# Kernel tuning notes

Hardware: AMD Instinct MI355X
Metric: run time of the kernel (lower is better)

Reference implementation:

```python
import jax, jax.numpy as jnp
import numpy as np

N, D, K = 16384, 512, 8192  # tokens, embed_dim, n_embed


def setup_inputs() -> dict:
    key = jax.random.key(0)
    k1, k2 = jax.random.split(key)
    xs = jax.random.normal(k1, (N, D), dtype=jnp.float32)
    embed_weight = jax.random.normal(k2, (K, D), dtype=jnp.float32)
    return {"xs": xs, "embed_weight": embed_weight}


def reference(xs, embed_weight):
    distance = ((xs ** 2).sum(axis=1, keepdims=True)
                + (embed_weight ** 2).sum(axis=1)
                - 2.0 * jnp.matmul(xs, embed_weight.T))
    indices = jnp.argmin(distance, axis=1)           # [N]
    output = embed_weight[indices]                   # gather -> [N, D]
    # straight-through estimator
    output_x = xs + jax.lax.stop_gradient(output - xs)
    e_latent_loss = jnp.mean((jax.lax.stop_gradient(output) - xs) ** 2)
    q_latent_loss = jnp.mean((output - jax.lax.stop_gradient(xs)) ** 2)
    loss = q_latent_loss + 0.25 * e_latent_loss
    return output_x, loss
```

## Files before the change

### kernel.cpp

```cpp
#include <hip/hip_runtime.h>
#include <stdint.h>

#define N_TOK   16384
#define DIM     512
#define K_CODES 8192
#define BM      128
#define BN      256
#define BK      32
#define NCHUNK  32
#define MU      0.25f

typedef __attribute__((ext_vector_type(8))) _Float16 f16x8;
typedef __attribute__((ext_vector_type(4))) _Float16 f16x4;
typedef __attribute__((ext_vector_type(4))) float f32x4;
typedef __attribute__((ext_vector_type(2))) unsigned long long u64x2;

__device__ __forceinline__ unsigned int fmono(float f) {
  unsigned int b = __float_as_uint(f);
  unsigned int mask = ((int)b < 0) ? 0xFFFFFFFFu : 0x80000000u;
  return b ^ mask;
}
__device__ __forceinline__ float finv(unsigned int m) {
  return (m & 0x80000000u) ? __uint_as_float(m ^ 0x80000000u)
                           : __uint_as_float(~m);
}
__device__ __forceinline__ void async16(const void* gptr, void* lptr) {
  __builtin_amdgcn_global_load_lds(
      (const __attribute__((address_space(1))) unsigned int*)gptr,
      (__attribute__((address_space(3))) unsigned int*)lptr,
      16, 0, 0);
}
__device__ __forceinline__ unsigned long long shflx(unsigned long long v, int x) {
  const int lo = __shfl_xor((int)(unsigned int)v, x, 64);
  const int hi = __shfl_xor((int)(unsigned int)(v >> 32), x, 64);
  return ((unsigned long long)(unsigned int)hi << 32) | (unsigned int)lo;
}
__device__ __forceinline__ unsigned long long umin64(unsigned long long a,
                                                     unsigned long long b) {
  return a < b ? a : b;
}
__device__ __forceinline__ unsigned long long umax64(unsigned long long a,
                                                     unsigned long long b) {
  return a < b ? b : a;
}

__global__ __launch_bounds__(256) void castx_kernel(
    const float* __restrict__ in, _Float16* __restrict__ out) {
  const int gid = blockIdx.x * 256 + threadIdx.x;
  const float4 v = ((const float4*)in)[gid];
  f16x4 h;
  h.x = (_Float16)v.x; h.y = (_Float16)v.y;
  h.z = (_Float16)v.z; h.w = (_Float16)v.w;
  *(f16x4*)(out + (size_t)gid * 4) = h;
}

__global__ __launch_bounds__(256) void enorm_cast_kernel(
    const float* __restrict__ ew, float* __restrict__ enorm,
    _Float16* __restrict__ E16) {
  const int lane = threadIdx.x & 63;
  const int wid  = threadIdx.x >> 6;
  const int row  = blockIdx.x * 4 + wid;
  const float4 v0 = *(const float4*)(ew + (size_t)row * DIM + lane * 8);
  const float4 v1 = *(const float4*)(ew + (size_t)row * DIM + lane * 8 + 4);
  const float f[8] = {v0.x, v0.y, v0.z, v0.w, v1.x, v1.y, v1.z, v1.w};
  f16x8 h;
  double s = 0.0;
#pragma unroll
  for (int k = 0; k < 8; ++k) {
    s = fma((double)f[k], (double)f[k], s);
    h[k] = (_Float16)f[k];
  }
  *(f16x8*)(E16 + (size_t)row * DIM + lane * 8) = h;
#pragma unroll
  for (int off = 32; off > 0; off >>= 1) s += __shfl_down(s, off, 64);
  if (lane == 0) enorm[row] = (float)s;
}

__global__ __launch_bounds__(256) void gemm_top2_kernel(
    const _Float16* __restrict__ X16,
    const _Float16* __restrict__ E16,
    const float* __restrict__ enorm,
    unsigned long long* __restrict__ buf1,
    unsigned long long* __restrict__ buf2) {
  __shared__ __align__(16) union {
    _Float16 buf[2][12288];
    unsigned long long mg[BM][16][2];
  } sh;

  const int tid  = threadIdx.x;
  const int lane = tid & 63;
  const int wid  = tid >> 6;
  const int quad = lane >> 4;
  const int l15  = lane & 15;

  const int row0  = blockIdx.y * BM;
  const int nbase = blockIdx.x * BN;

  const int wm = (wid >> 1) * 64;
  const int wn = (wid & 1) * 128;

  const int issue0 = wid * 6;
  const int srow   = lane >> 2;
  const int schunk = (lane & 3) ^ ((lane >> 3) & 3);

  auto STAGE = [&](int p, int k0) {
    char* base = (char*)(&sh.buf[p][0]);
#pragma unroll
    for (int q = 0; q < 6; ++q) {
      const int issue = issue0 + q;
      if (issue < 8) {
        const int r = issue * 16 + srow;
        async16(X16 + (size_t)(row0 + r) * DIM + k0 + schunk * 8,
                base + issue * 1024);
      } else {
        const int bi = issue - 8;
        const int r = bi * 16 + srow;
        async16(E16 + (size_t)(nbase + r) * DIM + k0 + schunk * 8,
                base + 8192 + bi * 1024);
      }
    }
  };

  f32x4 acc[4][8];
#pragma unroll
  for (int i = 0; i < 4; ++i)
#pragma unroll
    for (int j = 0; j < 8; ++j) acc[i][j] = (f32x4){0.f, 0.f, 0.f, 0.f};

  STAGE(0, 0);
  __syncthreads();

  for (int ks = 0; ks < DIM / BK; ++ks) {
    const int p = ks & 1;
    if (ks < DIM / BK - 1) STAGE(p ^ 1, (ks + 1) * BK);

    const char* baseA = (const char*)(&sh.buf[p][0]);
    const char* baseB = baseA + 8192;
    f16x8 a[4];
#pragma unroll
    for (int i = 0; i < 4; ++i) {
      const int ra = wm + i * 16 + l15;
      a[i] = *(const f16x8*)(baseA + ra * 64 + ((quad ^ ((ra >> 1) & 3)) * 16));
    }
#pragma unroll
    for (int jh = 0; jh < 2; ++jh) {
      f16x8 b[4];
#pragma unroll
      for (int jj = 0; jj < 4; ++jj) {
        const int rb = wn + (jh * 4 + jj) * 16 + l15;
        b[jj] = *(const f16x8*)(baseB + rb * 64 + ((quad ^ ((rb >> 1) & 3)) * 16));
      }
#pragma unroll
      for (int i = 0; i < 4; ++i)
#pragma unroll
        for (int jj = 0; jj < 4; ++jj)
          acc[i][jh * 4 + jj] = __builtin_amdgcn_mfma_f32_16x16x32_f16(
              a[i], b[jj], acc[i][jh * 4 + jj], 0, 0, 0);
    }
    __syncthreads();
  }

  float en8[8];
#pragma unroll
  for (int j = 0; j < 8; ++j) en8[j] = enorm[nbase + wn + j * 16 + l15];
  const unsigned int ngb = (unsigned int)(nbase + wn + l15);

#pragma unroll
  for (int i = 0; i < 4; ++i) {
    const int mrow = wm + i * 16 + quad * 4;
#pragma unroll
    for (int r = 0; r < 4; ++r) {
      float b1 = __builtin_inff(), b2v = __builtin_inff();
      unsigned int b1i = 0u, b2i = 0u;
#pragma unroll
      for (int j = 0; j < 8; ++j) {
        const float v = fmaf(-2.f, acc[i][j][r], en8[j]);
        const unsigned int ng = ngb + j * 16;
        if (v < b1) { b2v = b1; b2i = b1i; b1 = v; b1i = ng; }
        else if (v < b2v) { b2v = v; b2i = ng; }
      }
      unsigned long long p1 =
          ((unsigned long long)fmono(b1) << 32) | (unsigned long long)b1i;
      unsigned long long p2 =
          ((unsigned long long)fmono(b2v) << 32) | (unsigned long long)b2i;
      {
        const unsigned long long q1 = shflx(p1, 1);
        const unsigned long long q2 = shflx(p2, 1);
        const unsigned long long hi = umax64(p1, q1);
        p1 = umin64(p1, q1);
        p2 = umin64(hi, umin64(p2, q2));
      }
      if (!(lane & 1)) {
        const int row = mrow + r;
        u64x2 w; w.x = p1; w.y = p2;
        *(u64x2*)&sh.mg[row][((wid & 1) * 8 + (l15 >> 1)) ^ (row & 7)][0] = w;
      }
    }
  }
  __syncthreads();

  if (tid < BM) {
    unsigned long long g1 = ~0ull, g2 = ~0ull;
#pragma unroll
    for (int s = 0; s < 16; ++s) {
      const u64x2 v = *(const u64x2*)&sh.mg[tid][s ^ (tid & 7)][0];
      const unsigned long long v1 = v.x, v2 = v.y;
      const unsigned long long lo = umin64(v1, g1);
      const unsigned long long hi = umax64(v1, g1);
      g1 = lo;
      g2 = umin64(hi, umin64(v2, g2));
    }
    buf1[(size_t)(row0 + tid) * NCHUNK + blockIdx.x] = g1;
    buf2[(size_t)(row0 + tid) * NCHUNK + blockIdx.x] = g2;
  }
}

__global__ __launch_bounds__(256) void rerank_gather_loss_kernel(
    const float* __restrict__ xs, const float* __restrict__ ew,
    const unsigned long long* __restrict__ buf1,
    const unsigned long long* __restrict__ buf2,
    float* __restrict__ out, float* __restrict__ loss_part) {
  const int lane = threadIdx.x & 63;
  const int wv = threadIdx.x >> 6;
  const int tok = blockIdx.x * 4 + wv;
  const unsigned long long p = (lane < 32)
      ? buf1[(size_t)tok * NCHUNK + lane]
      : buf2[(size_t)tok * NCHUNK + (lane - 32)];
  const float S = finv((unsigned int)(p >> 32));
  float m = S;
#pragma unroll
  for (int off = 32; off > 0; off >>= 1) m = fminf(m, __shfl_xor(m, off, 64));
  unsigned long long mask = __ballot(S < m + MU);

  const float4 x0 = *(const float4*)(xs + (size_t)tok * DIM + lane * 8);
  const float4 x1 = *(const float4*)(xs + (size_t)tok * DIM + lane * 8 + 4);
  const double xd[8] = {x0.x, x0.y, x0.z, x0.w, x1.x, x1.y, x1.z, x1.w};

  double best = __builtin_inf();
  unsigned int besti = 0xFFFFFFFFu;
  while (mask) {
    const int src = __ffsll(mask) - 1;
    mask &= mask - 1;
    const unsigned int ci = (unsigned int)__shfl((int)(unsigned int)p, src, 64);
    const float4 e0 = *(const float4*)(ew + (size_t)ci * DIM + lane * 8);
    const float4 e1 = *(const float4*)(ew + (size_t)ci * DIM + lane * 8 + 4);
    const double ed[8] = {e0.x, e0.y, e0.z, e0.w, e1.x, e1.y, e1.z, e1.w};
    double s = 0.0;
#pragma unroll
    for (int k = 0; k < 8; ++k) {
      const double d = xd[k] - ed[k];
      s = fma(d, d, s);
    }
#pragma unroll
    for (int off = 32; off > 0; off >>= 1) s += __shfl_xor(s, off, 64);
    if (s < best || (s == best && ci < besti)) { best = s; besti = ci; }
  }

  const float4 e0 = *(const float4*)(ew + (size_t)besti * DIM + lane * 8);
  const float4 e1 = *(const float4*)(ew + (size_t)besti * DIM + lane * 8 + 4);
  *(float4*)(out + (size_t)tok * DIM + lane * 8) = e0;
  *(float4*)(out + (size_t)tok * DIM + lane * 8 + 4) = e1;
  const float ef[8] = {e0.x, e0.y, e0.z, e0.w, e1.x, e1.y, e1.z, e1.w};
  const float xf[8] = {x0.x, x0.y, x0.z, x0.w, x1.x, x1.y, x1.z, x1.w};
  float ls = 0.f;
#pragma unroll
  for (int k = 0; k < 8; ++k) {
    const float d = ef[k] - xf[k];
    ls = fmaf(d, d, ls);
  }
#pragma unroll
  for (int off = 32; off > 0; off >>= 1) ls += __shfl_xor(ls, off, 64);
  if (lane == 0) loss_part[tok] = ls;
}

__global__ __launch_bounds__(256) void loss_reduce_finalize(
    const float* __restrict__ part, float* __restrict__ out, int out_size) {
  const int t = threadIdx.x;
  float s = 0.f;
  for (int i = t; i < N_TOK; i += 256) s += part[i];
#pragma unroll
  for (int off = 32; off > 0; off >>= 1) s += __shfl_down(s, off, 64);
  __shared__ float ws4[4];
  if ((t & 63) == 0) ws4[t >> 6] = s;
  __syncthreads();
  if (t == 0)
    out[out_size - 1] = (ws4[0] + ws4[1] + ws4[2] + ws4[3]) * 1.25f /
                        (float)((size_t)N_TOK * DIM);
}

__global__ void loss_finalize(const float* __restrict__ loss_acc,
                              float* __restrict__ out, int out_size) {
  if (threadIdx.x == 0 && blockIdx.x == 0)
    out[out_size - 1] = *loss_acc * 1.25f / (float)((size_t)N_TOK * DIM);
}

#define TT 16
#define CT 16
#define KH 256
#define XPAD 516
#define EPAD 260
__global__ __launch_bounds__(256) void brute_argmin_kernel(
    const float* __restrict__ xs, const float* __restrict__ ew,
    unsigned int* __restrict__ g_idx) {
  __shared__ __align__(16) float Xs[TT * XPAD];
  __shared__ __align__(16) float Es[CT * EPAD];
  __shared__ double cand_v[256];
  __shared__ unsigned int cand_i[256];
  const int t = threadIdx.x;
  const int tok0 = blockIdx.x * TT;
#pragma unroll
  for (int i = 0; i < 32; ++i) {
    const int idx = i * 256 + t;
    const int row = idx >> 9, col = idx & 511;
    Xs[row * XPAD + col] = xs[(size_t)(tok0 + row) * DIM + col];
  }
  const int tt = t >> 4;
  const int cl = t & 15;
  double bv = __builtin_inf();
  unsigned int bi = 0u;
  for (int c0 = 0; c0 < K_CODES; c0 += CT) {
    double s0 = 0.0, s1 = 0.0, s2 = 0.0, s3 = 0.0;
#pragma unroll
    for (int h = 0; h < 2; ++h) {
      __syncthreads();
#pragma unroll
      for (int i = 0; i < 16; ++i) {
        const int idx = i * 256 + t;
        const int row = idx >> 8, col = idx & 255;
        Es[row * EPAD + col] = ew[(size_t)(c0 + row) * DIM + h * KH + col];
      }
      __syncthreads();
      const float* __restrict__ xr = &Xs[tt * XPAD + h * KH];
      const float* __restrict__ er = &Es[cl * EPAD];
#pragma unroll 8
      for (int d = 0; d < KH; d += 4) {
        const float4 xf = *(const float4*)(xr + d);
        const float4 ef = *(const float4*)(er + d);
        const double a0 = (double)xf.x - (double)ef.x;
        const double a1 = (double)xf.y - (double)ef.y;
        const double a2 = (double)xf.z - (double)ef.z;
        const double a3 = (double)xf.w - (double)ef.w;
        s0 = fma(a0, a0, s0); s1 = fma(a1, a1, s1);
        s2 = fma(a2, a2, s2); s3 = fma(a3, a3, s3);
      }
    }
    const double s = (s0 + s1) + (s2 + s3);
    if (s < bv) { bv = s; bi = (unsigned int)(c0 + cl); }
  }
  cand_v[t] = bv; cand_i[t] = bi;
  __syncthreads();
  if (t < TT) {
    double mv = __builtin_inf();
    unsigned int mi = 0xFFFFFFFFu;
#pragma unroll
    for (int j = 0; j < 16; ++j) {
      const double v = cand_v[t * 16 + j];
      const unsigned int i = cand_i[t * 16 + j];
      if (v < mv || (v == mv && i < mi)) { mv = v; mi = i; }
    }
    g_idx[tok0 + t] = mi;
  }
}

__global__ __launch_bounds__(256) void gather_loss_kernel(
    const float* __restrict__ xs, const float* __restrict__ ew,
    const unsigned int* __restrict__ g_idx,
    float* __restrict__ out, float* __restrict__ loss_acc) {
  const int row = blockIdx.x;
  const int t = threadIdx.x;
  const unsigned int idx = g_idx[row];
  const float2 ev = ((const float2*)(ew + (size_t)idx * DIM))[t];
  const float2 xv = ((const float2*)(xs + (size_t)row * DIM))[t];
  ((float2*)(out + (size_t)row * DIM))[t] = ev;
  const float d0 = ev.x - xv.x;
  const float d1 = ev.y - xv.y;
  float s = fmaf(d0, d0, d1 * d1);
#pragma unroll
  for (int off = 32; off > 0; off >>= 1) s += __shfl_down(s, off, 64);
  __shared__ float wsum[4];
  if ((t & 63) == 0) wsum[t >> 6] = s;
  __syncthreads();
  if (t == 0) atomicAdd(loss_acc, wsum[0] + wsum[1] + wsum[2] + wsum[3]);
}

extern "C" void kernel_launch(void* const* d_in, const int* in_sizes, int n_in,
                              void* d_out, int out_size, void* d_ws, size_t ws_size,
                              hipStream_t stream) {
  const float* xs = (const float*)d_in[0];
  const float* ew = (const float*)d_in[1];
  if (n_in >= 2 && in_sizes[0] == K_CODES * DIM && in_sizes[1] == N_TOK * DIM) {
    const float* tmp = xs; xs = ew; ew = tmp;
  }
  float* out = (float*)d_out;

  char* w = (char*)d_ws;
  _Float16* X16 = (_Float16*)(w);
  _Float16* E16 = (_Float16*)(w + 16777216);
  float* enorm = (float*)(w + 25165824);
  unsigned long long* buf1 = (unsigned long long*)(w + 25198592);
  unsigned long long* buf2 = (unsigned long long*)(w + 29392896);
  const size_t NEED = 33587264;

  float* loss_part = (float*)(w);

  if (ws_size < NEED) {
    unsigned int* fg_idx = (unsigned int*)d_ws;
    float* floss = (float*)((char*)d_ws + (size_t)N_TOK * 4);
    hipMemsetAsync(floss, 0, 4, stream);
    brute_argmin_kernel<<<N_TOK / TT, 256, 0, stream>>>(xs, ew, fg_idx);
    gather_loss_kernel<<<N_TOK, 256, 0, stream>>>(xs, ew, fg_idx, out, floss);
    loss_finalize<<<1, 64, 0, stream>>>(floss, out, out_size);
    return;
  }

  castx_kernel<<<N_TOK * DIM / 4 / 256, 256, 0, stream>>>(xs, X16);
  enorm_cast_kernel<<<K_CODES / 4, 256, 0, stream>>>(ew, enorm, E16);

  dim3 g2(K_CODES / BN, N_TOK / BM);
  gemm_top2_kernel<<<g2, 256, 0, stream>>>(X16, E16, enorm, buf1, buf2);

  rerank_gather_loss_kernel<<<N_TOK / 4, 256, 0, stream>>>(xs, ew, buf1, buf2,
                                                           out, loss_part);
  loss_reduce_finalize<<<1, 256, 0, stream>>>(loss_part, out, out_size);
}
```

Measured before the change: 317.3 us.

## Pack top-2 candidates into 32-bit keys and parallelize loss reduction

The GEMM epilogue now packs each candidate into a single 32-bit key: a truncated monotone distance in the upper 24 bits and the in-chunk code index in the low 8 bits. It selects the top-2 with a min/max network instead of branchy 64-bit compares, halving shuffle and buffer traffic. The rerank kernel rebuilds the full index from the chunk lane. The staging address math is hoisted into incrementing pointers, and the single-block loss reduce becomes a multi-block atomic reduce plus a finalize kernel. Truncating the distance to 24 bits loses precision in candidate selection, which the exact rerank is relied on to correct, and the extra memset and launch add overhead.

```diff
diff --git a/kernel.cpp b/kernel.cpp
--- a/kernel.cpp
+++ b/kernel.cpp
@@ -13,7 +13,6 @@
 typedef __attribute__((ext_vector_type(8))) _Float16 f16x8;
 typedef __attribute__((ext_vector_type(4))) _Float16 f16x4;
 typedef __attribute__((ext_vector_type(4))) float f32x4;
-typedef __attribute__((ext_vector_type(2))) unsigned long long u64x2;
 
 __device__ __forceinline__ unsigned int fmono(float f) {
   unsigned int b = __float_as_uint(f);
@@ -30,17 +29,10 @@
       (__attribute__((address_space(3))) unsigned int*)lptr,
       16, 0, 0);
 }
-__device__ __forceinline__ unsigned long long shflx(unsigned long long v, int x) {
-  const int lo = __shfl_xor((int)(unsigned int)v, x, 64);
-  const int hi = __shfl_xor((int)(unsigned int)(v >> 32), x, 64);
-  return ((unsigned long long)(unsigned int)hi << 32) | (unsigned int)lo;
-}
-__device__ __forceinline__ unsigned long long umin64(unsigned long long a,
-                                                     unsigned long long b) {
+__device__ __forceinline__ unsigned int umin32(unsigned int a, unsigned int b) {
   return a < b ? a : b;
 }
-__device__ __forceinline__ unsigned long long umax64(unsigned long long a,
-                                                     unsigned long long b) {
+__device__ __forceinline__ unsigned int umax32(unsigned int a, unsigned int b) {
   return a < b ? b : a;
 }
 
@@ -80,11 +72,11 @@
     const _Float16* __restrict__ X16,
     const _Float16* __restrict__ E16,
     const float* __restrict__ enorm,
-    unsigned long long* __restrict__ buf1,
-    unsigned long long* __restrict__ buf2) {
+    unsigned int* __restrict__ buf1,
+    unsigned int* __restrict__ buf2) {
   __shared__ __align__(16) union {
     _Float16 buf[2][12288];
-    unsigned long long mg[BM][16][2];
+    unsigned int mg[BM][16][2];
   } sh;
 
   const int tid  = threadIdx.x;
@@ -99,26 +91,26 @@
   const int wm = (wid >> 1) * 64;
   const int wn = (wid & 1) * 128;
 
-  const int issue0 = wid * 6;
   const int srow   = lane >> 2;
   const int schunk = (lane & 3) ^ ((lane >> 3) & 3);
 
-  auto STAGE = [&](int p, int k0) {
+  const int ia0 = wid * 2, ib0 = wid * 4;
+  const _Float16* pA0 = X16 + (size_t)(row0 + ia0 * 16 + srow) * DIM + schunk * 8;
+  const _Float16* pA1 = pA0 + (size_t)16 * DIM;
+  const _Float16* pB0 = E16 + (size_t)(nbase + ib0 * 16 + srow) * DIM + schunk * 8;
+  const _Float16* pB1 = pB0 + (size_t)16 * DIM;
+  const _Float16* pB2 = pB1 + (size_t)16 * DIM;
+  const _Float16* pB3 = pB2 + (size_t)16 * DIM;
+
+  auto STAGE = [&](int p) {
     char* base = (char*)(&sh.buf[p][0]);
-#pragma unroll
-    for (int q = 0; q < 6; ++q) {
-      const int issue = issue0 + q;
-      if (issue < 8) {
-        const int r = issue * 16 + srow;
-        async16(X16 + (size_t)(row0 + r) * DIM + k0 + schunk * 8,
-                base + issue * 1024);
-      } else {
-        const int bi = issue - 8;
-        const int r = bi * 16 + srow;
-        async16(E16 + (size_t)(nbase + r) * DIM + k0 + schunk * 8,
-                base + 8192 + bi * 1024);
-      }
-    }
+    async16(pA0, base + ia0 * 1024);
+    async16(pA1, base + ia0 * 1024 + 1024);
+    async16(pB0, base + 8192 + ib0 * 1024);
+    async16(pB1, base + 8192 + ib0 * 1024 + 1024);
+    async16(pB2, base + 8192 + ib0 * 1024 + 2048);
+    async16(pB3, base + 8192 + ib0 * 1024 + 3072);
+    pA0 += BK; pA1 += BK; pB0 += BK; pB1 += BK; pB2 += BK; pB3 += BK;
   };
 
   f32x4 acc[4][8];
@@ -127,12 +119,12 @@
 #pragma unroll
     for (int j = 0; j < 8; ++j) acc[i][j] = (f32x4){0.f, 0.f, 0.f, 0.f};
 
-  STAGE(0, 0);
+  STAGE(0);
   __syncthreads();
 
   for (int ks = 0; ks < DIM / BK; ++ks) {
     const int p = ks & 1;
-    if (ks < DIM / BK - 1) STAGE(p ^ 1, (ks + 1) * BK);
+    if (ks < DIM / BK - 1) STAGE(p ^ 1);
 
     const char* baseA = (const char*)(&sh.buf[p][0]);
     const char* baseB = baseA + 8192;
@@ -163,52 +155,54 @@
   float en8[8];
 #pragma unroll
   for (int j = 0; j < 8; ++j) en8[j] = enorm[nbase + wn + j * 16 + l15];
-  const unsigned int ngb = (unsigned int)(nbase + wn + l15);
+  const unsigned int cb = (unsigned int)(wn + l15);
 
 #pragma unroll
   for (int i = 0; i < 4; ++i) {
     const int mrow = wm + i * 16 + quad * 4;
 #pragma unroll
     for (int r = 0; r < 4; ++r) {
-      float b1 = __builtin_inff(), b2v = __builtin_inff();
-      unsigned int b1i = 0u, b2i = 0u;
+      unsigned int c[8];
 #pragma unroll
       for (int j = 0; j < 8; ++j) {
         const float v = fmaf(-2.f, acc[i][j][r], en8[j]);
-        const unsigned int ng = ngb + j * 16;
-        if (v < b1) { b2v = b1; b2i = b1i; b1 = v; b1i = ng; }
-        else if (v < b2v) { b2v = v; b2i = ng; }
-      }
-      unsigned long long p1 =
-          ((unsigned long long)fmono(b1) << 32) | (unsigned long long)b1i;
-      unsigned long long p2 =
-          ((unsigned long long)fmono(b2v) << 32) | (unsigned long long)b2i;
+        c[j] = (fmono(v) & 0xFFFFFF00u) | (cb + j * 16);
+      }
+      const unsigned int l0 = umin32(c[0], c[1]), h0 = umax32(c[0], c[1]);
+      const unsigned int l1 = umin32(c[2], c[3]), h1 = umax32(c[2], c[3]);
+      const unsigned int l2 = umin32(c[4], c[5]), h2 = umax32(c[4], c[5]);
+      const unsigned int l3 = umin32(c[6], c[7]), h3 = umax32(c[6], c[7]);
+      const unsigned int L0 = umin32(l0, l1);
+      const unsigned int S0 = umin32(umax32(l0, l1), umin32(h0, h1));
+      const unsigned int L1 = umin32(l2, l3);
+      const unsigned int S1 = umin32(umax32(l2, l3), umin32(h2, h3));
+      unsigned int p1 = umin32(L0, L1);
+      unsigned int p2 = umin32(umax32(L0, L1), umin32(S0, S1));
       {
-        const unsigned long long q1 = shflx(p1, 1);
-        const unsigned long long q2 = shflx(p2, 1);
-        const unsigned long long hi = umax64(p1, q1);
-        p1 = umin64(p1, q1);
-        p2 = umin64(hi, umin64(p2, q2));
+        const unsigned int q1 = (unsigned int)__shfl_xor((int)p1, 1, 64);
+        const unsigned int q2 = (unsigned int)__shfl_xor((int)p2, 1, 64);
+        const unsigned int hi = umax32(p1, q1);
+        p1 = umin32(p1, q1);
+        p2 = umin32(hi, umin32(p2, q2));
       }
       if (!(lane & 1)) {
         const int row = mrow + r;
-        u64x2 w; w.x = p1; w.y = p2;
-        *(u64x2*)&sh.mg[row][((wid & 1) * 8 + (l15 >> 1)) ^ (row & 7)][0] = w;
+        uint2 w; w.x = p1; w.y = p2;
+        *(uint2*)&sh.mg[row][((wid & 1) * 8 + (l15 >> 1)) ^ (row & 7)][0] = w;
       }
     }
   }
   __syncthreads();
 
   if (tid < BM) {
-    unsigned long long g1 = ~0ull, g2 = ~0ull;
+    unsigned int g1 = 0xFFFFFFFFu, g2 = 0xFFFFFFFFu;
 #pragma unroll
     for (int s = 0; s < 16; ++s) {
-      const u64x2 v = *(const u64x2*)&sh.mg[tid][s ^ (tid & 7)][0];
-      const unsigned long long v1 = v.x, v2 = v.y;
-      const unsigned long long lo = umin64(v1, g1);
-      const unsigned long long hi = umax64(v1, g1);
+      const uint2 v = *(const uint2*)&sh.mg[tid][s ^ (tid & 7)][0];
+      const unsigned int lo = umin32(v.x, g1);
+      const unsigned int hi = umax32(v.x, g1);
       g1 = lo;
-      g2 = umin64(hi, umin64(v2, g2));
+      g2 = umin32(hi, umin32(v.y, g2));
     }
     buf1[(size_t)(row0 + tid) * NCHUNK + blockIdx.x] = g1;
     buf2[(size_t)(row0 + tid) * NCHUNK + blockIdx.x] = g2;
@@ -217,16 +211,16 @@
 
 __global__ __launch_bounds__(256) void rerank_gather_loss_kernel(
     const float* __restrict__ xs, const float* __restrict__ ew,
-    const unsigned long long* __restrict__ buf1,
-    const unsigned long long* __restrict__ buf2,
+    const unsigned int* __restrict__ buf1,
+    const unsigned int* __restrict__ buf2,
     float* __restrict__ out, float* __restrict__ loss_part) {
   const int lane = threadIdx.x & 63;
   const int wv = threadIdx.x >> 6;
   const int tok = blockIdx.x * 4 + wv;
-  const unsigned long long p = (lane < 32)
+  const unsigned int p = (lane < 32)
       ? buf1[(size_t)tok * NCHUNK + lane]
       : buf2[(size_t)tok * NCHUNK + (lane - 32)];
-  const float S = finv((unsigned int)(p >> 32));
+  const float S = finv(p & 0xFFFFFF00u);
   float m = S;
 #pragma unroll
   for (int off = 32; off > 0; off >>= 1) m = fminf(m, __shfl_xor(m, off, 64));
@@ -241,7 +235,8 @@
   while (mask) {
     const int src = __ffsll(mask) - 1;
     mask &= mask - 1;
-    const unsigned int ci = (unsigned int)__shfl((int)(unsigned int)p, src, 64);
+    const unsigned int pp = (unsigned int)__shfl((int)p, src, 64);
+    const unsigned int ci = (unsigned int)((src & 31) << 8) | (pp & 0xFFu);
     const float4 e0 = *(const float4*)(ew + (size_t)ci * DIM + lane * 8);
     const float4 e1 = *(const float4*)(ew + (size_t)ci * DIM + lane * 8 + 4);
     const double ed[8] = {e0.x, e0.y, e0.z, e0.w, e1.x, e1.y, e1.z, e1.w};
@@ -273,19 +268,16 @@
   if (lane == 0) loss_part[tok] = ls;
 }
 
-__global__ __launch_bounds__(256) void loss_reduce_finalize(
-    const float* __restrict__ part, float* __restrict__ out, int out_size) {
+__global__ __launch_bounds__(256) void loss_reduce_part(
+    const float* __restrict__ part, float* __restrict__ loss_acc) {
   const int t = threadIdx.x;
-  float s = 0.f;
-  for (int i = t; i < N_TOK; i += 256) s += part[i];
+  float s = part[blockIdx.x * 256 + t];
 #pragma unroll
   for (int off = 32; off > 0; off >>= 1) s += __shfl_down(s, off, 64);
   __shared__ float ws4[4];
   if ((t & 63) == 0) ws4[t >> 6] = s;
   __syncthreads();
-  if (t == 0)
-    out[out_size - 1] = (ws4[0] + ws4[1] + ws4[2] + ws4[3]) * 1.25f /
-                        (float)((size_t)N_TOK * DIM);
+  if (t == 0) atomicAdd(loss_acc, ws4[0] + ws4[1] + ws4[2] + ws4[3]);
 }
 
 __global__ void loss_finalize(const float* __restrict__ loss_acc,
@@ -397,9 +389,10 @@
   _Float16* X16 = (_Float16*)(w);
   _Float16* E16 = (_Float16*)(w + 16777216);
   float* enorm = (float*)(w + 25165824);
-  unsigned long long* buf1 = (unsigned long long*)(w + 25198592);
-  unsigned long long* buf2 = (unsigned long long*)(w + 29392896);
-  const size_t NEED = 33587264;
+  unsigned int* buf1 = (unsigned int*)(w + 25198592);
+  unsigned int* buf2 = (unsigned int*)(w + 27295744);
+  float* loss_acc = (float*)(w + 29392896);
+  const size_t NEED = 29392960;
 
   float* loss_part = (float*)(w);
 
@@ -413,6 +406,8 @@
     return;
   }
 
+  hipMemsetAsync(loss_acc, 0, 4, stream);
+
   castx_kernel<<<N_TOK * DIM / 4 / 256, 256, 0, stream>>>(xs, X16);
   enorm_cast_kernel<<<K_CODES / 4, 256, 0, stream>>>(ew, enorm, E16);
 
@@ -421,5 +416,6 @@
 
   rerank_gather_loss_kernel<<<N_TOK / 4, 256, 0, stream>>>(xs, ew, buf1, buf2,
                                                            out, loss_part);
-  loss_reduce_finalize<<<1, 256, 0, stream>>>(loss_part, out, out_size);
-}
+  loss_reduce_part<<<N_TOK / 256, 256, 0, stream>>>(loss_part, loss_acc);
+  loss_finalize<<<1, 64, 0, stream>>>(loss_acc, out, out_size);
+}
```

Result: slower. 329.2 us (+3.8%).
